# Optimization experiments

Measured on AMD Instinct MI355X. Metric: run time of the kernel, lower is better.

Reference implementation:

```python
import jax, jax.numpy as jnp
import numpy as np

NUM_HEADS = 16
NUM_BUCKETS = 32
MAX_DISTANCE = 128


def _relative_position_bucket(relative_position, num_buckets=NUM_BUCKETS, max_distance=MAX_DISTANCE):
    # bidirectional=True (encoder self-attention)
    nb = num_buckets // 2  # 16
    buckets = (relative_position > 0).astype(jnp.int32) * nb
    rp = jnp.abs(relative_position)
    max_exact = nb // 2  # 8
    is_small = rp < max_exact
    # log-spaced bins for large distances; clamp arg of log to >=1 to avoid log(0)
    rp_f = jnp.maximum(rp, 1).astype(jnp.float32)
    large = max_exact + (
        jnp.log(rp_f / max_exact) / np.log(max_distance / max_exact) * (nb - max_exact)
    ).astype(jnp.int32)
    large = jnp.minimum(large, nb - 1)
    return buckets + jnp.where(is_small, rp, large)


def setup_inputs() -> dict:
    key = jax.random.key(0)
    ks = jax.random.split(key, 6)
    B, L, D = 2, 2048, 1024
    scale = 0.02  # keep activations in a sane range
    return {
        "hidden_states": jax.random.normal(ks[0], (B, L, D), dtype=jnp.float32),
        "Wq": jax.random.normal(ks[1], (D, D), dtype=jnp.float32) * scale,
        "Wk": jax.random.normal(ks[2], (D, D), dtype=jnp.float32) * scale,
        "Wv": jax.random.normal(ks[3], (D, D), dtype=jnp.float32) * scale,
        "Wo": jax.random.normal(ks[4], (D, D), dtype=jnp.float32) * scale,
        "bias_table": jax.random.normal(ks[5], (NUM_BUCKETS, NUM_HEADS), dtype=jnp.float32),
    }


def reference(hidden_states, Wq, Wk, Wv, Wo, bias_table):
    B, L, D = hidden_states.shape
    H = NUM_HEADS
    hd = D // H

    # projections (nn.Linear: y = x @ W.T), split heads -> [B, H, L, hd]
    def proj(x, W):
        return (x @ W.T).reshape(B, L, H, hd).transpose(0, 2, 1, 3)

    q = proj(hidden_states, Wq)
    k = proj(hidden_states, Wk)
    v = proj(hidden_states, Wv)

    # T5 relative position bias: [1, H, L, L]
    ctx = jnp.arange(L)[:, None]
    mem = jnp.arange(L)[None, :]
    buckets = _relative_position_bucket(mem - ctx)  # [L, L]
    position_bias = bias_table[buckets].transpose(2, 0, 1)[None]  # [1, H, L, L]

    # NOTE: T5-style attention has NO 1/sqrt(hd) scaling
    scores = jnp.einsum("bhqd,bhkd->bhqk", q, k) + position_bias
    attn = jax.nn.softmax(scores.astype(jnp.float32), axis=-1).astype(scores.dtype)
    out = jnp.einsum("bhqk,bhkd->bhqd", attn, v)
    out = out.transpose(0, 2, 1, 3).reshape(B, L, D)
    out = out @ Wo.T
    return out, position_bias
```

## Files before the change

kernel.cpp:

```cpp
#include <hip/hip_runtime.h>
#include <cstdint>
#include <cmath>

typedef unsigned short ushort_t;
typedef __bf16 bf16x8 __attribute__((ext_vector_type(8)));
typedef float f32x4 __attribute__((ext_vector_type(4)));
typedef ushort_t us4 __attribute__((ext_vector_type(4)));
typedef ushort_t us8 __attribute__((ext_vector_type(8)));

#define MFMA16(a, b, c) __builtin_amdgcn_mfma_f32_16x16x32_bf16(a, b, c, 0, 0, 0)
#define LOG2E 1.4426950408889634f

__device__ __forceinline__ ushort_t f2bf(float f) {
    union { __bf16 h; ushort_t u; } cv;
    cv.h = (__bf16)f;
    return cv.u;
}

__device__ __forceinline__ void glds16(const ushort_t* g, ushort_t* s) {
    __builtin_amdgcn_global_load_lds(
        (const __attribute__((address_space(1))) void*)(g),
        (__attribute__((address_space(3))) void*)(s), 16, 0, 0);
}

__global__ void cast_all_k(const float* __restrict__ x, const float* __restrict__ wq,
                           const float* __restrict__ wk, const float* __restrict__ wv,
                           const float* __restrict__ wo, ushort_t* __restrict__ xb,
                           ushort_t* __restrict__ wb, unsigned char* __restrict__ lut) {
    int id = blockIdx.x, t = threadIdx.x;
    if (id == 8192) {
        for (int idx = t; idx < 4095; idx += 256) {
            int rel = idx - 2047;
            int bb = (rel > 0) ? 16 : 0;
            int rp = (rel < 0) ? -rel : rel;
            int add;
            if (rp < 8) {
                add = rp;
            } else {
                float lg = (float)::log((double)rp * 0.125);
                double tt = ((double)lg) / 2.772588722239781 * 8.0;
                int large = 8 + (int)tt;
                add = (large < 15) ? large : 15;
            }
            lut[idx] = (unsigned char)(bb + add);
        }
        return;
    }
    const float* src;
    ushort_t* dst;
    int idx;
    float scale = 1.0f;
    if (id < 4096) {
        src = x; dst = xb; idx = id * 256 + t;
    } else {
        int r = (id - 4096) >> 10;
        idx = ((id - 4096) & 1023) * 256 + t;
        src = (r == 0) ? wq : (r == 1) ? wk : (r == 2) ? wv : wo;
        dst = wb + (size_t)r * 1048576;
        if (r == 0) scale = LOG2E;
    }
    float4 v = ((const float4*)src)[idx];
    us4 o;
    o.x = f2bf(v.x * scale); o.y = f2bf(v.y * scale);
    o.z = f2bf(v.z * scale); o.w = f2bf(v.w * scale);
    ((us4*)dst)[idx] = o;
}

template <int MODE>
__global__ __launch_bounds__(256) void gemm_bt_k(const ushort_t* __restrict__ A,
                                                 const ushort_t* __restrict__ B0,
                                                 void* __restrict__ C0,
                                                 int M, int N, int K, long sB, long sC) {
    __shared__ ushort_t As[128 * 64];
    __shared__ ushort_t Bs[128 * 64];
    const int tid = threadIdx.x;
    const int l = tid & 63, w = tid >> 6;
    const int quad = l >> 4, lc = l & 15;
    const int wm = w >> 1, wn = w & 1;
    const int m0 = blockIdx.y * 128, n0 = blockIdx.x * 128;
    const ushort_t* B = B0 + (long)blockIdx.z * sB;

    f32x4 acc[4][4] = {};
    const int rA = l >> 3;
    const int cA = ((l & 7) ^ rA) * 8;

    for (int k0 = 0; k0 < K; k0 += 64) {
#pragma unroll
        for (int t = 0; t < 4; ++t) {
            int row = w * 32 + t * 8;
            glds16(A + (size_t)(m0 + row + rA) * K + k0 + cA, &As[row * 64]);
            glds16(B + (size_t)(n0 + row + rA) * K + k0 + cA, &Bs[row * 64]);
        }
        __syncthreads();
#pragma unroll
        for (int ko = 0; ko < 2; ++ko) {
            const int ch = (((ko * 4 + quad) ^ (lc & 7))) * 8;
            bf16x8 af[4], bfr[4];
#pragma unroll
            for (int mt = 0; mt < 4; ++mt)
                af[mt] = *(const bf16x8*)&As[(wm * 64 + mt * 16 + lc) * 64 + ch];
#pragma unroll
            for (int nt = 0; nt < 4; ++nt)
                bfr[nt] = *(const bf16x8*)&Bs[(wn * 64 + nt * 16 + lc) * 64 + ch];
#pragma unroll
            for (int mt = 0; mt < 4; ++mt)
#pragma unroll
                for (int nt = 0; nt < 4; ++nt)
                    acc[mt][nt] = MFMA16(af[mt], bfr[nt], acc[mt][nt]);
        }
        __syncthreads();
    }
#pragma unroll
    for (int mt = 0; mt < 4; ++mt) {
#pragma unroll
        for (int nt = 0; nt < 4; ++nt) {
            int col = n0 + wn * 64 + nt * 16 + lc;
#pragma unroll
            for (int r = 0; r < 4; ++r) {
                int row = m0 + wm * 64 + mt * 16 + quad * 4 + r;
                if constexpr (MODE == 1) {
                    ((float*)C0)[(size_t)row * N + col] = acc[mt][nt][r];
                } else if constexpr (MODE == 0) {
                    (((ushort_t*)C0) + (long)blockIdx.z * sC)[(size_t)row * N + col] = f2bf(acc[mt][nt][r]);
                } else {
                    ((ushort_t*)C0)[(size_t)(col >> 11) * 2097152 + (size_t)row * 2048 + (col & 2047)] =
                        f2bf(acc[mt][nt][r]);
                }
            }
        }
    }
}

__global__ __launch_bounds__(256, 2) void attn_k(const ushort_t* __restrict__ Qg,
                                                 const ushort_t* __restrict__ Kg,
                                                 const ushort_t* __restrict__ VTg,
                                                 ushort_t* __restrict__ Ctx,
                                                 const unsigned char* __restrict__ lut,
                                                 const float* __restrict__ table,
                                                 float* __restrict__ bias_out) {
    __shared__ ushort_t Kbuf[2][128 * 64];
    __shared__ ushort_t Pws[4 * 32 * 40];
    __shared__ float diag[2][256];

    const int tid = threadIdx.x, l = tid & 63, w = tid >> 6;
    const int quad = l >> 4, lc = l & 15;
    const int id = blockIdx.x;
    const int bh = id & 31, b = bh >> 4, h = bh & 15;
    const int q0 = (id >> 5) * 128;
    const size_t tokbase = (size_t)b * 2048;

    const int rK = l >> 3;
    const int cK = ((l & 7) ^ rK) * 8;

#pragma unroll
    for (int t = 0; t < 4; ++t) {
        int row0 = w * 32 + t * 8;
        glds16(Qg + (tokbase + q0 + row0 + rK) * 1024 + h * 64 + cK, &Kbuf[1][row0 * 64]);
        glds16(Kg + (tokbase + row0 + rK) * 1024 + h * 64 + cK, &Kbuf[0][row0 * 64]);
    }
    if (tid < 255) diag[0][tid] = table[(int)lut[tid + 1920 - q0] * 16 + h];
    __syncthreads();

    bf16x8 qf[2][2];
#pragma unroll
    for (int nt = 0; nt < 2; ++nt)
#pragma unroll
        for (int ko = 0; ko < 2; ++ko) {
            int row = w * 32 + nt * 16 + lc;
            int ch = ((ko * 4 + quad) ^ (lc & 7)) * 8;
            qf[nt][ko] = *(const bf16x8*)&Kbuf[1][row * 64 + ch];
        }
    __syncthreads();

    float mstate[2] = {-1e30f, -1e30f};
    float lstate[2] = {0.f, 0.f};
    f32x4 acco[4][2] = {};
    ushort_t* Pw = &Pws[w * 1280];
    const int cb0 = quad * 4 - (w * 32 + lc) + 127;
    const int cxor = lc & 3;
    const ushort_t* VTbase = VTg + (size_t)(b * 1024 + h * 64) * 2048;

    const int bjf = (tid & 15) * 4 + b * 64;
    const int big = tid >> 4;

    for (int kt = 0; kt < 16; ++kt) {
        const int j0 = kt * 128;
        const int cur = kt & 1, nxt = cur ^ 1;
        const ushort_t* Kc = Kbuf[cur];
        const float* dc = diag[cur];

        if (kt < 15) {
            const int jn = j0 + 128;
#pragma unroll
            for (int t = 0; t < 4; ++t) {
                int row0 = w * 32 + t * 8;
                glds16(Kg + (tokbase + jn + row0 + rK) * 1024 + h * 64 + cK, &Kbuf[nxt][row0 * 64]);
            }
            if (tid < 255) diag[nxt][tid] = table[(int)lut[jn - q0 + tid + 1920] * 16 + h];
        }

        bf16x8 vf[4][4];
#pragma unroll
        for (int kk = 0; kk < 4; ++kk)
#pragma unroll
            for (int dt = 0; dt < 4; ++dt)
                vf[kk][dt] = *(const bf16x8*)(VTbase + (size_t)(dt * 16 + lc) * 2048 +
                                              j0 + kk * 32 + quad * 8);

        {
            float* outp = bias_out + ((size_t)h * 2048 + q0) * 2048 + j0;
#pragma unroll
            for (int rr = 0; rr < 8; ++rr) {
                int il = big + 16 * rr;
                int d0 = bjf - il + 127;
                f32x4 v;
                v[0] = dc[d0]; v[1] = dc[d0 + 1]; v[2] = dc[d0 + 2]; v[3] = dc[d0 + 3];
                __builtin_nontemporal_store(v, (f32x4*)(outp + (size_t)il * 2048 + bjf));
            }
        }

        f32x4 accs[8][2] = {};
#pragma unroll
        for (int ko = 0; ko < 2; ++ko) {
            const int ch = ((ko * 4 + quad) ^ (lc & 7)) * 8;
#pragma unroll
            for (int mt = 0; mt < 8; ++mt) {
                bf16x8 kf = *(const bf16x8*)&Kc[(mt * 16 + lc) * 64 + ch];
                accs[mt][0] = MFMA16(kf, qf[0][ko], accs[mt][0]);
                accs[mt][1] = MFMA16(kf, qf[1][ko], accs[mt][1]);
            }
        }

        float dprev[4], dcur[4];
#pragma unroll
        for (int r = 0; r < 4; ++r) dprev[r] = dc[cb0 - 16 + r];
#pragma unroll
        for (int mt = 0; mt < 8; ++mt) {
#pragma unroll
            for (int r = 0; r < 4; ++r) dcur[r] = dc[cb0 + mt * 16 + r];
#pragma unroll
            for (int r = 0; r < 4; ++r) {
                accs[mt][0][r] = fmaf(dcur[r], LOG2E, accs[mt][0][r]);
                accs[mt][1][r] = fmaf(dprev[r], LOG2E, accs[mt][1][r]);
            }
#pragma unroll
            for (int r = 0; r < 4; ++r) dprev[r] = dcur[r];
        }

#pragma unroll
        for (int nt = 0; nt < 2; ++nt) {
            float mx = accs[0][nt][0];
#pragma unroll
            for (int mt = 0; mt < 8; ++mt)
#pragma unroll
                for (int r = 0; r < 4; ++r) mx = fmaxf(mx, accs[mt][nt][r]);
            mx = fmaxf(mx, __shfl_xor(mx, 16, 64));
            mx = fmaxf(mx, __shfl_xor(mx, 32, 64));
            float mo = mstate[nt], mn = fmaxf(mo, mx);
            float alpha = __builtin_amdgcn_exp2f(mo - mn);
            mstate[nt] = mn;
            float rs = 0.f;
#pragma unroll
            for (int mt = 0; mt < 8; ++mt)
#pragma unroll
                for (int r = 0; r < 4; ++r) {
                    float p = __builtin_amdgcn_exp2f(accs[mt][nt][r] - mn);
                    accs[mt][nt][r] = p;
                    rs += p;
                }
            rs += __shfl_xor(rs, 16, 64);
            rs += __shfl_xor(rs, 32, 64);
            lstate[nt] = lstate[nt] * alpha + rs;
#pragma unroll
            for (int dt = 0; dt < 4; ++dt) acco[dt][nt] *= alpha;
        }

#pragma unroll
        for (int kk = 0; kk < 4; ++kk) {
#pragma unroll
            for (int half = 0; half < 2; ++half) {
                int mt = kk * 2 + half;
                int c = half * 2 + (quad >> 1);
                int coff = ((c ^ cxor) * 8 + (quad & 1) * 4);
#pragma unroll
                for (int nt = 0; nt < 2; ++nt) {
                    us4 o;
#pragma unroll
                    for (int r = 0; r < 4; ++r) o[r] = f2bf(accs[mt][nt][r]);
                    *(us4*)&Pw[(nt * 16 + lc) * 40 + coff] = o;
                }
            }
            bf16x8 pf[2];
#pragma unroll
            for (int nt = 0; nt < 2; ++nt)
                pf[nt] = *(const bf16x8*)&Pw[(nt * 16 + lc) * 40 + (quad ^ cxor) * 8];
#pragma unroll
            for (int dt = 0; dt < 4; ++dt)
#pragma unroll
                for (int nt = 0; nt < 2; ++nt)
                    acco[dt][nt] = MFMA16(vf[kk][dt], pf[nt], acco[dt][nt]);
        }
        if (kt < 15) __syncthreads();
    }

#pragma unroll
    for (int nt = 0; nt < 2; ++nt) {
        float inv = 1.0f / lstate[nt];
        size_t row = tokbase + q0 + w * 32 + nt * 16 + lc;
#pragma unroll
        for (int dt = 0; dt < 4; ++dt) {
            us4 o;
#pragma unroll
            for (int r = 0; r < 4; ++r) o[r] = f2bf(acco[dt][nt][r] * inv);
            *(us4*)&Ctx[row * 1024 + h * 64 + dt * 16 + quad * 4] = o;
        }
    }
}

extern "C" void kernel_launch(void* const* d_in, const int* in_sizes, int n_in,
                              void* d_out, int out_size, void* d_ws, size_t ws_size,
                              hipStream_t stream) {
    const float* hidden = (const float*)d_in[0];
    const float* Wq = (const float*)d_in[1];
    const float* Wk = (const float*)d_in[2];
    const float* Wv = (const float*)d_in[3];
    const float* Wo = (const float*)d_in[4];
    const float* table = (const float*)d_in[5];

    char* ws = (char*)d_ws;
    ushort_t* Xb  = (ushort_t*)(ws);
    ushort_t* Wb  = (ushort_t*)(ws + 8388608);
    ushort_t* Qg  = (ushort_t*)(ws + 16777216);
    ushort_t* Kgp = (ushort_t*)(ws + 25165824);
    ushort_t* VTg = (ushort_t*)(ws + 33554432);
    ushort_t* Ctx = (ushort_t*)(ws + 41943040);
    unsigned char* lutp = (unsigned char*)(ws + 50331648);

    float* out0 = (float*)d_out;
    float* out1 = out0 + 4194304;

    cast_all_k<<<8193, 256, 0, stream>>>(hidden, Wq, Wk, Wv, Wo, Xb, Wb, lutp);

    gemm_bt_k<0><<<dim3(8, 32, 2), 256, 0, stream>>>(Xb, Wb, (void*)Qg,
                                                     4096, 1024, 1024, 1048576, 4194304);
    gemm_bt_k<2><<<dim3(32, 8, 1), 256, 0, stream>>>(Wb + 2097152, Xb, (void*)VTg,
                                                     1024, 4096, 1024, 0, 0);
    attn_k<<<dim3(512), 256, 0, stream>>>(Qg, Kgp, VTg, Ctx, lutp, table, out1);
    gemm_bt_k<1><<<dim3(8, 32, 1), 256, 0, stream>>>(Ctx, Wb + 3145728, (void*)out0,
                                                     4096, 1024, 1024, 0, 0);
}
```

Measured before the change: 426.0 us.

## Merge QK and V^T projection launches; add MFMA priority and lazy softmax rescale

Replaces the two projection GEMM launches with one 768-block kernel that computes the Q/K tiles and the transposed-V tiles in a single grid. This removes a launch and lets the two GEMMs fill the GPU together. The attention kernel raises wave priority around its MFMA sections and skips the online-softmax rescale when the wave-wide max grows by 8 or less in log2 units. It also reorganises the max and sum reductions into trees. The deferred rescale lets exponentials reach up to 2^8, which relies on that margin to stay accurate in fp32 and bf16.

Result: slower. 484.6 us (+13.8%).

```diff
diff --git a/kernel.cpp b/kernel.cpp
--- a/kernel.cpp
+++ b/kernel.cpp
@@ -131,6 +131,83 @@
     }
 }
 
+__global__ __launch_bounds__(256) void gemm_qkvt_k(const ushort_t* __restrict__ Xb,
+                                                   const ushort_t* __restrict__ Wb,
+                                                   ushort_t* __restrict__ QKg,
+                                                   ushort_t* __restrict__ VTg) {
+    __shared__ ushort_t As[128 * 64];
+    __shared__ ushort_t Bs[128 * 64];
+    const int tid = threadIdx.x;
+    const int l = tid & 63, w = tid >> 6;
+    const int quad = l >> 4, lc = l & 15;
+    const int wm = w >> 1, wn = w & 1;
+    const int id = blockIdx.x;
+
+    const ushort_t* A;
+    const ushort_t* B;
+    int m0, n0, z = 0;
+    bool vt;
+    if (id < 512) {
+        vt = false; z = id >> 8;
+        int r = id & 255;
+        m0 = (r >> 3) * 128; n0 = (r & 7) * 128;
+        A = Xb; B = Wb + z * 1048576;
+    } else {
+        vt = true;
+        int r = id - 512;
+        m0 = (r >> 5) * 128; n0 = (r & 31) * 128;
+        A = Wb + 2097152; B = Xb;
+    }
+
+    f32x4 acc[4][4] = {};
+    const int rA = l >> 3;
+    const int cA = ((l & 7) ^ rA) * 8;
+
+    for (int k0 = 0; k0 < 1024; k0 += 64) {
+#pragma unroll
+        for (int t = 0; t < 4; ++t) {
+            int row = w * 32 + t * 8;
+            glds16(A + (size_t)(m0 + row + rA) * 1024 + k0 + cA, &As[row * 64]);
+            glds16(B + (size_t)(n0 + row + rA) * 1024 + k0 + cA, &Bs[row * 64]);
+        }
+        __syncthreads();
+#pragma unroll
+        for (int ko = 0; ko < 2; ++ko) {
+            const int ch = (((ko * 4 + quad) ^ (lc & 7))) * 8;
+            bf16x8 af[4], bfr[4];
+#pragma unroll
+            for (int mt = 0; mt < 4; ++mt)
+                af[mt] = *(const bf16x8*)&As[(wm * 64 + mt * 16 + lc) * 64 + ch];
+#pragma unroll
+            for (int nt = 0; nt < 4; ++nt)
+                bfr[nt] = *(const bf16x8*)&Bs[(wn * 64 + nt * 16 + lc) * 64 + ch];
+#pragma unroll
+            for (int mt = 0; mt < 4; ++mt)
+#pragma unroll
+                for (int nt = 0; nt < 4; ++nt)
+                    acc[mt][nt] = MFMA16(af[mt], bfr[nt], acc[mt][nt]);
+        }
+        __syncthreads();
+    }
+#pragma unroll
+    for (int mt = 0; mt < 4; ++mt) {
+#pragma unroll
+        for (int nt = 0; nt < 4; ++nt) {
+            int col = n0 + wn * 64 + nt * 16 + lc;
+#pragma unroll
+            for (int r = 0; r < 4; ++r) {
+                int row = m0 + wm * 64 + mt * 16 + quad * 4 + r;
+                if (!vt) {
+                    QKg[(size_t)z * 4194304 + (size_t)row * 1024 + col] = f2bf(acc[mt][nt][r]);
+                } else {
+                    VTg[(size_t)(col >> 11) * 2097152 + (size_t)row * 2048 + (col & 2047)] =
+                        f2bf(acc[mt][nt][r]);
+                }
+            }
+        }
+    }
+}
+
 __global__ __launch_bounds__(256, 2) void attn_k(const ushort_t* __restrict__ Qg,
                                                  const ushort_t* __restrict__ Kg,
                                                  const ushort_t* __restrict__ VTg,
@@ -220,6 +297,7 @@
         }
 
         f32x4 accs[8][2] = {};
+        __builtin_amdgcn_s_setprio(1);
 #pragma unroll
         for (int ko = 0; ko < 2; ++ko) {
             const int ch = ((ko * 4 + quad) ^ (lc & 7)) * 8;
@@ -230,6 +308,7 @@
                 accs[mt][1] = MFMA16(kf, qf[1][ko], accs[mt][1]);
             }
         }
+        __builtin_amdgcn_s_setprio(0);
 
         float dprev[4], dcur[4];
 #pragma unroll
@@ -249,30 +328,48 @@
 
 #pragma unroll
         for (int nt = 0; nt < 2; ++nt) {
-            float mx = accs[0][nt][0];
+            float m8[8];
 #pragma unroll
             for (int mt = 0; mt < 8; ++mt)
-#pragma unroll
-                for (int r = 0; r < 4; ++r) mx = fmaxf(mx, accs[mt][nt][r]);
+                m8[mt] = fmaxf(fmaxf(accs[mt][nt][0], accs[mt][nt][1]),
+                               fmaxf(accs[mt][nt][2], accs[mt][nt][3]));
+            float mx = fmaxf(fmaxf(fmaxf(m8[0], m8[1]), fmaxf(m8[2], m8[3])),
+                             fmaxf(fmaxf(m8[4], m8[5]), fmaxf(m8[6], m8[7])));
             mx = fmaxf(mx, __shfl_xor(mx, 16, 64));
             mx = fmaxf(mx, __shfl_xor(mx, 32, 64));
-            float mo = mstate[nt], mn = fmaxf(mo, mx);
-            float alpha = __builtin_amdgcn_exp2f(mo - mn);
-            mstate[nt] = mn;
-            float rs = 0.f;
-#pragma unroll
-            for (int mt = 0; mt < 8; ++mt)
-#pragma unroll
-                for (int r = 0; r < 4; ++r) {
-                    float p = __builtin_amdgcn_exp2f(accs[mt][nt][r] - mn);
-                    accs[mt][nt][r] = p;
-                    rs += p;
-                }
+
+            float mo = mstate[nt];
+            bool defer = __all(mx - mo <= 8.0f);
+            float mn = mo, alpha = 1.0f;
+            if (!defer) {
+                mn = fmaxf(mo, mx);
+                alpha = __builtin_amdgcn_exp2f(mo - mn);
+                mstate[nt] = mn;
+            }
+
+            float s8[8];
+#pragma unroll
+            for (int mt = 0; mt < 8; ++mt) {
+                float p0 = __builtin_amdgcn_exp2f(accs[mt][nt][0] - mn);
+                float p1 = __builtin_amdgcn_exp2f(accs[mt][nt][1] - mn);
+                float p2 = __builtin_amdgcn_exp2f(accs[mt][nt][2] - mn);
+                float p3 = __builtin_amdgcn_exp2f(accs[mt][nt][3] - mn);
+                accs[mt][nt][0] = p0; accs[mt][nt][1] = p1;
+                accs[mt][nt][2] = p2; accs[mt][nt][3] = p3;
+                s8[mt] = (p0 + p1) + (p2 + p3);
+            }
+            float rs = ((s8[0] + s8[1]) + (s8[2] + s8[3])) +
+                       ((s8[4] + s8[5]) + (s8[6] + s8[7]));
             rs += __shfl_xor(rs, 16, 64);
             rs += __shfl_xor(rs, 32, 64);
-            lstate[nt] = lstate[nt] * alpha + rs;
-#pragma unroll
-            for (int dt = 0; dt < 4; ++dt) acco[dt][nt] *= alpha;
+
+            if (defer) {
+                lstate[nt] += rs;
+            } else {
+                lstate[nt] = lstate[nt] * alpha + rs;
+#pragma unroll
+                for (int dt = 0; dt < 4; ++dt) acco[dt][nt] *= alpha;
+            }
         }
 
 #pragma unroll
@@ -294,11 +391,13 @@
 #pragma unroll
             for (int nt = 0; nt < 2; ++nt)
                 pf[nt] = *(const bf16x8*)&Pw[(nt * 16 + lc) * 40 + (quad ^ cxor) * 8];
+            __builtin_amdgcn_s_setprio(1);
 #pragma unroll
             for (int dt = 0; dt < 4; ++dt)
 #pragma unroll
                 for (int nt = 0; nt < 2; ++nt)
                     acco[dt][nt] = MFMA16(vf[kk][dt], pf[nt], acco[dt][nt]);
+            __builtin_amdgcn_s_setprio(0);
         }
         if (kt < 15) __syncthreads();
     }
@@ -341,10 +440,8 @@
 
     cast_all_k<<<8193, 256, 0, stream>>>(hidden, Wq, Wk, Wv, Wo, Xb, Wb, lutp);
 
-    gemm_bt_k<0><<<dim3(8, 32, 2), 256, 0, stream>>>(Xb, Wb, (void*)Qg,
-                                                     4096, 1024, 1024, 1048576, 4194304);
-    gemm_bt_k<2><<<dim3(32, 8, 1), 256, 0, stream>>>(Wb + 2097152, Xb, (void*)VTg,
-                                                     1024, 4096, 1024, 0, 0);
+    gemm_qkvt_k<<<768, 256, 0, stream>>>(Xb, Wb, Qg, VTg);
+
     attn_k<<<dim3(512), 256, 0, stream>>>(Qg, Kgp, VTg, Ctx, lutp, table, out1);
     gemm_bt_k<1><<<dim3(8, 32, 1), 256, 0, stream>>>(Ctx, Wb + 3145728, (void*)out0,
                                                      4096, 1024, 1024, 0, 0);
```
